# Kernel optimization log

Measured on AMD Instinct MI355X. Metric: run time of the kernel, lower is better.

## Reference

```python
import jax, jax.numpy as jnp
from jax import lax
import numpy as np

T, B, IN, H = 512, 256, 128, 512
TAU_MIN, TAU_MAX, DT = 0.2, 2.0, 0.1


def setup_inputs() -> dict:
    key = jax.random.key(0)
    ks = jax.random.split(key, 7)
    s_zh = 1.0 / np.sqrt(IN + H)  # torch Linear default init scale (fan_in)
    s_h = 1.0 / np.sqrt(H)
    return {
        "x_seq": jax.random.normal(ks[0], (T, B, IN), dtype=jnp.float32),
        "Wc": jax.random.uniform(ks[1], (IN + H, H), jnp.float32, -s_zh, s_zh),
        "bc": jax.random.uniform(ks[2], (H,), jnp.float32, -s_zh, s_zh),
        "Wt": jax.random.uniform(ks[3], (IN + H, H), jnp.float32, -s_zh, s_zh),
        "bt": jax.random.uniform(ks[4], (H,), jnp.float32, -s_zh, s_zh),
        "Wo": jax.random.uniform(ks[5], (H, 1), jnp.float32, -s_h, s_h),
        "bo": jax.random.uniform(ks[6], (1,), jnp.float32, -s_h, s_h),
    }


def reference(x_seq, Wc, bc, Wt, bt, Wo, bo):
    # Liquid time-constant RNN: sequential scan over T timesteps.
    def step(h, x_t):
        z = jnp.concatenate([x_t, h], axis=-1)           # [B, IN+H]
        candidate = jnp.tanh(z @ Wc + bc)                # [B, H]
        tau = TAU_MIN + jax.nn.sigmoid(z @ Wt + bt) * (TAU_MAX - TAU_MIN)
        h_next = h + DT * (-h + candidate) / tau         # ODE Euler update
        y_t = h_next @ Wo + bo                           # [B, 1]
        return h_next, (y_t, tau)

    h0 = jnp.zeros((x_seq.shape[1], Wc.shape[1]), dtype=x_seq.dtype)
    _, (y_seq, tau_seq) = lax.scan(step, h0, x_seq)
    return y_seq, tau_seq
```

## Files before the change

kernel.cpp:

```cpp
#include <hip/hip_runtime.h>
#include <stdint.h>

#define T_STEPS 512
#define BATCH   256
#define INP     128
#define HID     512
#define BGN     16
#define CGN     8
#define RB      16
#define CB      64
#define ZP      648

typedef float f32x4 __attribute__((ext_vector_type(4)));
typedef short s16x8 __attribute__((ext_vector_type(8)));
typedef unsigned short u16;
typedef unsigned int   u32;
typedef unsigned long long u64;

__device__ __forceinline__ u32 f2bf(float f) {
  union { float f; u32 u; } v; v.f = f;
  return (v.u + 0x7fffu + ((v.u >> 16) & 1u)) >> 16;
}


__global__ __launch_bounds__(256, 1)
void liquid_persistent(const float* __restrict__ x_seq,
                       const float* __restrict__ Wc, const float* __restrict__ bc,
                       const float* __restrict__ Wt, const float* __restrict__ bt,
                       const float* __restrict__ Wo, const float* __restrict__ bo,
                       float* __restrict__ y_out, float* __restrict__ tau_out,
                       u16* __restrict__ hb)
{
  const int tid  = threadIdx.x;
  const int l    = tid & 63;
  const int w    = tid >> 6;
  const int quad = l >> 4;
  const int ln   = l & 15;
  const int bg   = blockIdx.x & (BGN - 1);
  const int cg   = blockIdx.x >> 4;
  const int R0   = bg * RB;
  const int C0   = cg * CB;
  const int cn   = C0 + w * 16 + ln;

  __shared__ u16 zS[RB][ZP];

  s16x8 wfC[20], wfT[20];
#pragma unroll
  for (int kt = 0; kt < 20; ++kt) {
#pragma unroll
    for (int j = 0; j < 8; ++j) {
      int k = kt * 32 + quad * 8 + j;
      wfC[kt][j] = (short)f2bf(Wc[k * HID + cn]);
      wfT[kt][j] = (short)f2bf(Wt[k * HID + cn]);
    }
  }

  const float bcv = bc[cn], btv = bt[cn], wov = Wo[cn];
  const float boadd = (cg == 0 && w == 0) ? bo[0] : 0.0f;
  float hm[4] = {0.f, 0.f, 0.f, 0.f};

  const int xrow = tid >> 4;
  const int xseg = tid & 15;

  int ii[7];
#pragma unroll
  for (int jx = 0; jx < 7; ++jx) ii[jx] = jx + (jx >= cg ? 1 : 0);

  const size_t rowq = HID / 4;
  u64* hbase = (u64*)(void*)hb;
  const size_t myrow = (size_t)(R0 + xrow) * rowq;

  {
    const float* xp = x_seq + ((size_t)0 * BATCH + R0 + xrow) * INP + xseg * 8;
    float4 a = *(const float4*)xp;
    float4 b = *(const float4*)(xp + 4);
    u64 w0 = (u64)f2bf(a.x) | ((u64)f2bf(a.y) << 16) |
             ((u64)f2bf(a.z) << 32) | ((u64)f2bf(a.w) << 48);
    u64 w1 = (u64)f2bf(b.x) | ((u64)f2bf(b.y) << 16) |
             ((u64)f2bf(b.z) << 32) | ((u64)f2bf(b.w) << 48);
    *(u64*)&zS[xrow][xseg * 8]     = w0;
    *(u64*)&zS[xrow][xseg * 8 + 4] = w1;
  }
  __syncthreads();

  for (int t = 0; t < T_STEPS; ++t) {
    const u64* rbase = hbase + (size_t)(t & 3) * BATCH * rowq + myrow + xseg;

    u64 tmp[7];
    if (t > 0) {
#pragma unroll
      for (int jx = 0; jx < 7; ++jx)
        tmp[jx] = __hip_atomic_load(rbase + ii[jx] * 16, __ATOMIC_RELAXED,
                                    __HIP_MEMORY_SCOPE_AGENT);
    }

    f32x4 aC0 = {0.f,0.f,0.f,0.f}, aC1 = {0.f,0.f,0.f,0.f};
    f32x4 aT0 = {0.f,0.f,0.f,0.f}, aT1 = {0.f,0.f,0.f,0.f};
    const u16* zb = &zS[ln][quad * 8];
    {
      s16x8 a0 = *(const s16x8*)(zb);
      s16x8 a1 = *(const s16x8*)(zb + 32);
      s16x8 a2 = *(const s16x8*)(zb + 64);
      s16x8 a3 = *(const s16x8*)(zb + 96);
      aC0 = __builtin_amdgcn_mfma_f32_16x16x32_bf16(a0, wfC[0], aC0, 0,0,0);
      aT0 = __builtin_amdgcn_mfma_f32_16x16x32_bf16(a0, wfT[0], aT0, 0,0,0);
      aC1 = __builtin_amdgcn_mfma_f32_16x16x32_bf16(a1, wfC[1], aC1, 0,0,0);
      aT1 = __builtin_amdgcn_mfma_f32_16x16x32_bf16(a1, wfT[1], aT1, 0,0,0);
      aC0 = __builtin_amdgcn_mfma_f32_16x16x32_bf16(a2, wfC[2], aC0, 0,0,0);
      aT0 = __builtin_amdgcn_mfma_f32_16x16x32_bf16(a2, wfT[2], aT0, 0,0,0);
      aC1 = __builtin_amdgcn_mfma_f32_16x16x32_bf16(a3, wfC[3], aC1, 0,0,0);
      aT1 = __builtin_amdgcn_mfma_f32_16x16x32_bf16(a3, wfT[3], aT1, 0,0,0);
    }

    u64 hv[7];
    if (t == 0) {
#pragma unroll
      for (int jx = 0; jx < 7; ++jx) hv[jx] = 0;
    } else {
      bool need[7];
      int pending = 0;
#pragma unroll
      for (int jx = 0; jx < 7; ++jx) {
        u64 v = tmp[jx];
        bool ok = ((u32)v != 0xFFFFFFFFu) && ((u32)(v >> 32) != 0xFFFFFFFFu);
        hv[jx] = v;
        need[jx] = !ok;
        pending += ok ? 0 : 1;
      }
      while (pending) {
#pragma unroll
        for (int jx = 0; jx < 7; ++jx)
          if (need[jx])
            tmp[jx] = __hip_atomic_load(rbase + ii[jx] * 16, __ATOMIC_RELAXED,
                                        __HIP_MEMORY_SCOPE_AGENT);
#pragma unroll
        for (int jx = 0; jx < 7; ++jx)
          if (need[jx]) {
            u64 v = tmp[jx];
            if (((u32)v != 0xFFFFFFFFu) && ((u32)(v >> 32) != 0xFFFFFFFFu)) {
              hv[jx] = v;
              need[jx] = false;
              --pending;
            }
          }
      }
    }

    {
      u64* pp = hbase + (size_t)((t + 2) & 3) * BATCH * rowq + myrow
              + (C0 / 4 + xseg);
      __hip_atomic_store(pp, ~0ull, __ATOMIC_RELAXED, __HIP_MEMORY_SCOPE_AGENT);
    }

    const int tn = (t + 1 < T_STEPS) ? t + 1 : t;
    const float* xp = x_seq + ((size_t)tn * BATCH + R0 + xrow) * INP + xseg * 8;
    float4 xr0 = *(const float4*)xp;
    float4 xr1 = *(const float4*)(xp + 4);

#pragma unroll
    for (int jx = 0; jx < 7; ++jx)
      *(u64*)&zS[xrow][INP + (ii[jx] * 16 + xseg) * 4] = hv[jx];
#pragma unroll
    for (int r = 0; r < 4; ++r)
      zS[quad * 4 + r][INP + cn] = (u16)f2bf(hm[r]);

    __syncthreads();

#pragma unroll
    for (int kt = 4; kt < 20; kt += 2) {
      s16x8 a0 = *(const s16x8*)(zb + kt * 32);
      s16x8 a1 = *(const s16x8*)(zb + kt * 32 + 32);
      aC0 = __builtin_amdgcn_mfma_f32_16x16x32_bf16(a0, wfC[kt],   aC0, 0,0,0);
      aT0 = __builtin_amdgcn_mfma_f32_16x16x32_bf16(a0, wfT[kt],   aT0, 0,0,0);
      aC1 = __builtin_amdgcn_mfma_f32_16x16x32_bf16(a1, wfC[kt+1], aC1, 0,0,0);
      aT1 = __builtin_amdgcn_mfma_f32_16x16x32_bf16(a1, wfT[kt+1], aT1, 0,0,0);
    }
    aC0 += aC1;
    aT0 += aT1;

    {
      u64 w0 = (u64)f2bf(xr0.x) | ((u64)f2bf(xr0.y) << 16) |
               ((u64)f2bf(xr0.z) << 32) | ((u64)f2bf(xr0.w) << 48);
      u64 w1 = (u64)f2bf(xr1.x) | ((u64)f2bf(xr1.y) << 16) |
               ((u64)f2bf(xr1.z) << 32) | ((u64)f2bf(xr1.w) << 48);
      *(u64*)&zS[xrow][xseg * 8]     = w0;
      *(u64*)&zS[xrow][xseg * 8 + 4] = w1;
    }

    float tauv[4];
#pragma unroll
    for (int r = 0; r < 4; ++r) {
      float pc = aC0[r] + bcv;
      float pt = aT0[r] + btv;
      pc = fminf(fmaxf(pc, -20.f), 20.f);
      float e  = __expf(2.f * pc);
      float cand = (e - 1.f) / (e + 1.f);
      float tau  = 0.2f + 1.8f / (1.f + __expf(-pt));
      hm[r] += 0.1f * (cand - hm[r]) / tau;
      tauv[r] = tau;
    }

    asm volatile("s_waitcnt vmcnt(0)" ::: "memory");

#pragma unroll
    for (int r = 0; r < 4; ++r) {
      u32 bits = f2bf(hm[r]);
      u32 b0   = bits | ((u32)__shfl_xor((int)bits, 1) << 16);
      u64 q    = (u64)b0 | ((u64)(u32)__shfl_xor((int)b0, 2) << 32);
      if (!(ln & 3)) {
        u64* hp = hbase + (size_t)((t + 1) & 3) * BATCH * rowq
                + (size_t)(R0 + quad * 4 + r) * rowq + (cn / 4);
        __hip_atomic_store(hp, q, __ATOMIC_RELAXED, __HIP_MEMORY_SCOPE_AGENT);
      }
    }

    __syncthreads();

#pragma unroll
    for (int r = 0; r < 4; ++r)
      __builtin_nontemporal_store(
          tauv[r],
          &tau_out[((size_t)t * BATCH + R0 + quad * 4 + r) * HID + cn]);
#pragma unroll
    for (int r = 0; r < 4; ++r) {
      float py = hm[r] * wov;
      py += __shfl_down(py, 8, 16);
      py += __shfl_down(py, 4, 16);
      py += __shfl_down(py, 2, 16);
      py += __shfl_down(py, 1, 16);
      if (ln == 0)
        atomicAdd(&y_out[t * BATCH + R0 + quad * 4 + r], py + boadd);
    }
  }
}

extern "C" void kernel_launch(void* const* d_in, const int* in_sizes, int n_in,
                              void* d_out, int out_size, void* d_ws, size_t ws_size,
                              hipStream_t stream) {
  (void)in_sizes; (void)n_in; (void)out_size; (void)ws_size;
  const float* x_seq = (const float*)d_in[0];
  const float* Wc    = (const float*)d_in[1];
  const float* bc    = (const float*)d_in[2];
  const float* Wt    = (const float*)d_in[3];
  const float* bt    = (const float*)d_in[4];
  const float* Wo    = (const float*)d_in[5];
  const float* bo    = (const float*)d_in[6];

  float* y_out   = (float*)d_out;
  float* tau_out = (float*)d_out + (size_t)T_STEPS * BATCH;

  const size_t HB_BYTES = (size_t)4 * BATCH * HID * sizeof(u16);
  u16* hb = (u16*)d_ws;

  hipMemsetAsync(d_out, 0, (size_t)T_STEPS * BATCH * sizeof(float), stream);
  hipMemsetAsync(d_ws, 0xFF, HB_BYTES, stream);

  liquid_persistent<<<dim3(BGN * CGN), dim3(256), 0, stream>>>(
      x_seq, Wc, bc, Wt, bt, Wo, bo, y_out, tau_out, hb);
}
```

Measured before the change: 2.071 ms.

## Compute y from gathered full hidden row instead of atomic partial sums

Each block now computes the output y for two batch rows per step from the full bf16 hidden state already gathered in shared memory, one step late. An extra loop iteration handles the final step. This replaces the per-block atomicAdd of partial dot products and removes the memset of y_out. The cost is an extra iteration, a shared-memory reduction, and y now being computed from bf16-rounded h rather than fp32 h, which slightly changes precision.

```diff
diff --git a/kernel.cpp b/kernel.cpp
--- a/kernel.cpp
+++ b/kernel.cpp
@@ -20,6 +20,11 @@
 __device__ __forceinline__ u32 f2bf(float f) {
   union { float f; u32 u; } v; v.f = f;
   return (v.u + 0x7fffu + ((v.u >> 16) & 1u)) >> 16;
+}
+
+__device__ __forceinline__ float bf2f(u16 b) {
+  union { u32 u; float f; } v; v.u = ((u32)b) << 16;
+  return v.f;
 }
 
 
@@ -43,6 +48,7 @@
   const int cn   = C0 + w * 16 + ln;
 
   __shared__ u16 zS[RB][ZP];
+  __shared__ float ypS[4];
 
   s16x8 wfC[20], wfT[20];
 #pragma unroll
@@ -55,12 +61,16 @@
     }
   }
 
-  const float bcv = bc[cn], btv = bt[cn], wov = Wo[cn];
-  const float boadd = (cg == 0 && w == 0) ? bo[0] : 0.0f;
+  const float bcv = bc[cn], btv = bt[cn];
+  const float bov = bo[0];
   float hm[4] = {0.f, 0.f, 0.f, 0.f};
 
   const int xrow = tid >> 4;
   const int xseg = tid & 15;
+
+  const int yrow = 2 * cg + (w >> 1);
+  const int yc0  = (w & 1) * 256 + l * 4;
+  const float4 wo4 = *(const float4*)&Wo[yc0];
 
   int ii[7];
 #pragma unroll
@@ -83,7 +93,7 @@
   }
   __syncthreads();
 
-  for (int t = 0; t < T_STEPS; ++t) {
+  for (int t = 0; t <= T_STEPS; ++t) {
     const u64* rbase = hbase + (size_t)(t & 3) * BATCH * rowq + myrow + xseg;
 
     u64 tmp[7];
@@ -97,7 +107,7 @@
     f32x4 aC0 = {0.f,0.f,0.f,0.f}, aC1 = {0.f,0.f,0.f,0.f};
     f32x4 aT0 = {0.f,0.f,0.f,0.f}, aT1 = {0.f,0.f,0.f,0.f};
     const u16* zb = &zS[ln][quad * 8];
-    {
+    if (t < T_STEPS) {
       s16x8 a0 = *(const s16x8*)(zb);
       s16x8 a1 = *(const s16x8*)(zb + 32);
       s16x8 a2 = *(const s16x8*)(zb + 64);
@@ -146,16 +156,19 @@
       }
     }
 
-    {
+    if (t < T_STEPS) {
       u64* pp = hbase + (size_t)((t + 2) & 3) * BATCH * rowq + myrow
               + (C0 / 4 + xseg);
       __hip_atomic_store(pp, ~0ull, __ATOMIC_RELAXED, __HIP_MEMORY_SCOPE_AGENT);
     }
 
-    const int tn = (t + 1 < T_STEPS) ? t + 1 : t;
-    const float* xp = x_seq + ((size_t)tn * BATCH + R0 + xrow) * INP + xseg * 8;
-    float4 xr0 = *(const float4*)xp;
-    float4 xr1 = *(const float4*)(xp + 4);
+    float4 xr0, xr1;
+    if (t < T_STEPS) {
+      const int tn = (t + 1 < T_STEPS) ? t + 1 : t;
+      const float* xp = x_seq + ((size_t)tn * BATCH + R0 + xrow) * INP + xseg * 8;
+      xr0 = *(const float4*)xp;
+      xr1 = *(const float4*)(xp + 4);
+    }
 
 #pragma unroll
     for (int jx = 0; jx < 7; ++jx)
@@ -166,70 +179,82 @@
 
     __syncthreads();
 
-#pragma unroll
-    for (int kt = 4; kt < 20; kt += 2) {
-      s16x8 a0 = *(const s16x8*)(zb + kt * 32);
-      s16x8 a1 = *(const s16x8*)(zb + kt * 32 + 32);
-      aC0 = __builtin_amdgcn_mfma_f32_16x16x32_bf16(a0, wfC[kt],   aC0, 0,0,0);
-      aT0 = __builtin_amdgcn_mfma_f32_16x16x32_bf16(a0, wfT[kt],   aT0, 0,0,0);
-      aC1 = __builtin_amdgcn_mfma_f32_16x16x32_bf16(a1, wfC[kt+1], aC1, 0,0,0);
-      aT1 = __builtin_amdgcn_mfma_f32_16x16x32_bf16(a1, wfT[kt+1], aT1, 0,0,0);
-    }
-    aC0 += aC1;
-    aT0 += aT1;
-
-    {
+    float tauv[4];
+    if (t < T_STEPS) {
+#pragma unroll
+      for (int kt = 4; kt < 20; kt += 2) {
+        s16x8 a0 = *(const s16x8*)(zb + kt * 32);
+        s16x8 a1 = *(const s16x8*)(zb + kt * 32 + 32);
+        aC0 = __builtin_amdgcn_mfma_f32_16x16x32_bf16(a0, wfC[kt],   aC0, 0,0,0);
+        aT0 = __builtin_amdgcn_mfma_f32_16x16x32_bf16(a0, wfT[kt],   aT0, 0,0,0);
+        aC1 = __builtin_amdgcn_mfma_f32_16x16x32_bf16(a1, wfC[kt+1], aC1, 0,0,0);
+        aT1 = __builtin_amdgcn_mfma_f32_16x16x32_bf16(a1, wfT[kt+1], aT1, 0,0,0);
+      }
+      aC0 += aC1;
+      aT0 += aT1;
+
       u64 w0 = (u64)f2bf(xr0.x) | ((u64)f2bf(xr0.y) << 16) |
                ((u64)f2bf(xr0.z) << 32) | ((u64)f2bf(xr0.w) << 48);
       u64 w1 = (u64)f2bf(xr1.x) | ((u64)f2bf(xr1.y) << 16) |
                ((u64)f2bf(xr1.z) << 32) | ((u64)f2bf(xr1.w) << 48);
       *(u64*)&zS[xrow][xseg * 8]     = w0;
       *(u64*)&zS[xrow][xseg * 8 + 4] = w1;
-    }
-
-    float tauv[4];
-#pragma unroll
-    for (int r = 0; r < 4; ++r) {
-      float pc = aC0[r] + bcv;
-      float pt = aT0[r] + btv;
-      pc = fminf(fmaxf(pc, -20.f), 20.f);
-      float e  = __expf(2.f * pc);
-      float cand = (e - 1.f) / (e + 1.f);
-      float tau  = 0.2f + 1.8f / (1.f + __expf(-pt));
-      hm[r] += 0.1f * (cand - hm[r]) / tau;
-      tauv[r] = tau;
-    }
-
-    asm volatile("s_waitcnt vmcnt(0)" ::: "memory");
-
-#pragma unroll
-    for (int r = 0; r < 4; ++r) {
-      u32 bits = f2bf(hm[r]);
-      u32 b0   = bits | ((u32)__shfl_xor((int)bits, 1) << 16);
-      u64 q    = (u64)b0 | ((u64)(u32)__shfl_xor((int)b0, 2) << 32);
-      if (!(ln & 3)) {
-        u64* hp = hbase + (size_t)((t + 1) & 3) * BATCH * rowq
-                + (size_t)(R0 + quad * 4 + r) * rowq + (cn / 4);
-        __hip_atomic_store(hp, q, __ATOMIC_RELAXED, __HIP_MEMORY_SCOPE_AGENT);
-      }
+
+#pragma unroll
+      for (int r = 0; r < 4; ++r) {
+        float pc = aC0[r] + bcv;
+        float pt = aT0[r] + btv;
+        pc = fminf(fmaxf(pc, -20.f), 20.f);
+        float e  = __expf(2.f * pc);
+        float cand = (e - 1.f) / (e + 1.f);
+        float tau  = 0.2f + 1.8f / (1.f + __expf(-pt));
+        hm[r] += 0.1f * (cand - hm[r]) / tau;
+        tauv[r] = tau;
+      }
+
+      asm volatile("s_waitcnt vmcnt(0)" ::: "memory");
+
+#pragma unroll
+      for (int r = 0; r < 4; ++r) {
+        u32 bits = f2bf(hm[r]);
+        u32 b0   = bits | ((u32)__shfl_xor((int)bits, 1) << 16);
+        u64 q    = (u64)b0 | ((u64)(u32)__shfl_xor((int)b0, 2) << 32);
+        if (!(ln & 3)) {
+          u64* hp = hbase + (size_t)((t + 1) & 3) * BATCH * rowq
+                  + (size_t)(R0 + quad * 4 + r) * rowq + (cn / 4);
+          __hip_atomic_store(hp, q, __ATOMIC_RELAXED, __HIP_MEMORY_SCOPE_AGENT);
+        }
+      }
+    }
+
+    if (t > 0) {
+      u64 hq = *(const u64*)&zS[yrow][INP + yc0];
+      float py = bf2f((u16)hq)          * wo4.x
+               + bf2f((u16)(hq >> 16))  * wo4.y
+               + bf2f((u16)(hq >> 32))  * wo4.z
+               + bf2f((u16)(hq >> 48))  * wo4.w;
+      py += __shfl_down(py, 32);
+      py += __shfl_down(py, 16);
+      py += __shfl_down(py, 8);
+      py += __shfl_down(py, 4);
+      py += __shfl_down(py, 2);
+      py += __shfl_down(py, 1);
+      if (l == 0) ypS[w] = py;
     }
 
     __syncthreads();
 
-#pragma unroll
-    for (int r = 0; r < 4; ++r)
-      __builtin_nontemporal_store(
-          tauv[r],
-          &tau_out[((size_t)t * BATCH + R0 + quad * 4 + r) * HID + cn]);
-#pragma unroll
-    for (int r = 0; r < 4; ++r) {
-      float py = hm[r] * wov;
-      py += __shfl_down(py, 8, 16);
-      py += __shfl_down(py, 4, 16);
-      py += __shfl_down(py, 2, 16);
-      py += __shfl_down(py, 1, 16);
-      if (ln == 0)
-        atomicAdd(&y_out[t * BATCH + R0 + quad * 4 + r], py + boadd);
+    if (t > 0 && tid < 2) {
+      float yv = ypS[tid * 2] + ypS[tid * 2 + 1] + bov;
+      y_out[(size_t)(t - 1) * BATCH + R0 + 2 * cg + tid] = yv;
+    }
+
+    if (t < T_STEPS) {
+#pragma unroll
+      for (int r = 0; r < 4; ++r)
+        __builtin_nontemporal_store(
+            tauv[r],
+            &tau_out[((size_t)t * BATCH + R0 + quad * 4 + r) * HID + cn]);
     }
   }
 }
@@ -252,7 +277,6 @@
   const size_t HB_BYTES = (size_t)4 * BATCH * HID * sizeof(u16);
   u16* hb = (u16*)d_ws;
 
-  hipMemsetAsync(d_out, 0, (size_t)T_STEPS * BATCH * sizeof(float), stream);
   hipMemsetAsync(d_ws, 0xFF, HB_BYTES, stream);
 
   liquid_persistent<<<dim3(BGN * CGN), dim3(256), 0, stream>>>(
```

After: 1.961 ms. 5.3% less time.
